# Kernel tuning notes

Measured on AMD Instinct MI355X. Metric: run time of the kernel, lower is better.

The kernel has to match this reference:

```python
import jax, jax.numpy as jnp
import numpy as np

EPS_BN = 1e-5
K_INTERP = 8
K_NEIGH = 16


def _bn(x, g, b):
    # BatchNorm1d in training mode: batch stats over rows (biased var), eps=1e-5
    m = x.mean(axis=0)
    v = x.var(axis=0)
    return (x - m) * jax.lax.rsqrt(v + EPS_BN) * g + b


def _dist(a, b):
    # a:(B,N,3), b:(B,M,3) -> Euclidean distance (B,N,M), computed via the
    # quadratic expansion (clamped at 0) instead of materializing (B,N,M,3)
    d2 = (jnp.sum(a * a, -1)[:, :, None] + jnp.sum(b * b, -1)[:, None, :]
          - 2.0 * jnp.einsum('bnc,bmc->bnm', a, b))
    return jnp.sqrt(jnp.maximum(d2, 0.0))


def _gather(feats, idx):
    # feats:(B,M,C), idx:(B,N,K) int -> (B,N,K,C)
    return jax.vmap(lambda f, i: f[i])(feats, idx)


def setup_inputs() -> dict:
    key = jax.random.key(0)
    B, N1, N2, DS, DD, DOUT = 4, 4096, 1024, 128, 64, 256
    ks = jax.random.split(key, 20)
    s = 0.02
    inp = {
        'p1': jax.random.uniform(ks[0], (B * N1, 3), jnp.float32),
        'x1': jax.random.normal(ks[1], (B * N1, DD), jnp.float32),
        'o1': (jnp.arange(B, dtype=jnp.int32) + 1) * N1,
        'p2': jax.random.uniform(ks[2], (B * N2, 3), jnp.float32),
        'x2': jax.random.normal(ks[3], (B * N2, DS), jnp.float32),
        'o2': (jnp.arange(B, dtype=jnp.int32) + 1) * N2,
        'batch_size': B,
        # dense_mlp: Linear(DD,DS) + BN
        'W_dense': jax.random.normal(ks[4], (DD, DS), jnp.float32) * s,
        'b_dense': jnp.zeros((DS,), jnp.float32),
        'g_dense': jnp.ones((DS,), jnp.float32),
        'bt_dense': jnp.zeros((DS,), jnp.float32),
        # CrossAttentionPointTransformerLayer (dim=DS, hidden_mult=1)
        'Wq': jax.random.normal(ks[5], (DS, DS), jnp.float32) * s,
        'Wk': jax.random.normal(ks[6], (DS, DS), jnp.float32) * s,
        'Wv': jax.random.normal(ks[7], (DS, DS), jnp.float32) * s,
        'W1': jax.random.normal(ks[8], (DS, DS), jnp.float32) * s,
        'b1': jnp.zeros((DS,), jnp.float32),
        'g1': jnp.ones((DS,), jnp.float32),
        'bt1': jnp.zeros((DS,), jnp.float32),
        'W2': jax.random.normal(ks[9], (DS, DS), jnp.float32) * s,
        'b2': jnp.zeros((DS,), jnp.float32),
        # output mlp: Linear(DS+DD, DOUT) + BN
        'W_out': jax.random.normal(ks[10], (DS + DD, DOUT), jnp.float32) * s,
        'b_out': jnp.zeros((DOUT,), jnp.float32),
        'g_out': jnp.ones((DOUT,), jnp.float32),
        'bt_out': jnp.zeros((DOUT,), jnp.float32),
    }
    return inp


def reference(p1, x1, o1, p2, x2, o2, batch_size,
              W_dense, b_dense, g_dense, bt_dense,
              Wq, Wk, Wv, W1, b1, g1, bt1, W2, b2,
              W_out, b_out, g_out, bt_out):
    B = int(batch_size)
    N1 = p1.shape[0] // B
    N2 = p2.shape[0] // B
    DS = x2.shape[-1]

    # dense_mlp
    x1_dense = jax.nn.relu(_bn(x1 @ W_dense + b_dense, g_dense, bt_dense))  # (B*N1, DS)

    # pointops.interpolation(p2, p1, x2, o2, o1, k=8): inverse-distance kNN interp
    p1b = p1.reshape(B, N1, 3)
    p2b = p2.reshape(B, N2, 3)
    x2b = x2.reshape(B, N2, DS)
    d12 = _dist(p1b, p2b)                       # (B,N1,N2)
    negd, idx = jax.lax.top_k(-d12, K_INTERP)   # k nearest in p2
    dknn = -negd
    recip = 1.0 / (dknn + 1e-8)
    w = recip / recip.sum(-1, keepdims=True)    # (B,N1,8)
    x2_interp = jnp.einsum('bnk,bnkc->bnc', w, _gather(x2b, idx))  # (B,N1,DS)

    # CrossAttentionPointTransformerLayer(x_e=x1_dense, x_r=x_d=x2_interp, pos=p1)
    x_e = x1_dense.reshape(B, N1, DS)
    q = x_e @ Wq
    k = x2_interp @ Wk
    v = x2_interp @ Wv
    rel_dist = _dist(p1b, p1b)                  # (B,N1,N1)
    _, nidx = jax.lax.top_k(-rel_dist, K_NEIGH) # 16 nearest neighbors
    kg = _gather(k, nidx)                        # (B,N1,16,DS)
    vg = _gather(v, nidx)
    xeg = _gather(x_e, nidx)
    qk_rel = q[:, :, None, :] - kg
    v2 = vg + xeg
    h = (qk_rel + xeg).reshape(-1, DS)           # (B*N1*16, DS)
    h = jax.nn.relu(_bn(h @ W1 + b1, g1, bt1))
    sim = (h @ W2 + b2).reshape(B, N1, K_NEIGH, DS)
    attn = jax.nn.softmax(sim, axis=-2)          # over neighbors
    agg = jnp.einsum('bnkc,bnkc->bnc', attn, v2).reshape(B * N1, DS)

    # output mlp
    x = jax.nn.relu(_bn(jnp.concatenate([agg, x1], axis=-1) @ W_out + b_out,
                        g_out, bt_out))
    return (p1, x, o1)
```

## Files before the change

kernel.cpp:

```cpp
#include <hip/hip_runtime.h>
#include <math.h>

#define BB 4
#define NN1 4096
#define NN2 1024
#define DS 128
#define DD 64
#define DOUT 256
#define M1 16384
#define MH 262144
#define KCAT 192
#define KI 8
#define KN 16

#define OUT_P1 49152
#define OUT_X  49152
#define OUT_O1 4243456


static const size_t OFF_WTS  = 16777216;
static const size_t OFF_TMP  = 33554432;
static const size_t OFF_XD   = OFF_TMP  + 2097152;
static const size_t OFF_XI   = OFF_XD   + 2097152;
static const size_t OFF_Q    = OFF_XI   + 2097152;
static const size_t OFF_K    = OFF_Q    + 2097152;
static const size_t OFF_V    = OFF_K    + 2097152;
static const size_t OFF_OUTP = OFF_V    + 2097152;
static const size_t OFF_NIDX = OFF_OUTP + 4194304;
static const size_t OFF_STAT = OFF_NIDX + 262144;
static const size_t OFF_P1Q  = OFF_STAT + 4096;
static const size_t OFF_P2Q  = OFF_P1Q  + 65536;
static const size_t OFF_P1S  = OFF_P2Q  + 16384;
static const size_t OFF_P2S  = OFF_P1S  + 65536;

#define WDH 0
#define WDL 8192
#define WQH 16384
#define WQL 32768
#define WKH 49152
#define WKL 65536
#define WVH 81920
#define WVL 98304
#define W1H 114688
#define W1L 131072
#define W2H 147456
#define W2L 163840
#define WOH 180224
#define WOL 229376

typedef __attribute__((ext_vector_type(8))) short short8;
typedef __attribute__((ext_vector_type(4))) float floatx4;
typedef __attribute__((ext_vector_type(2))) float float2v;

__device__ inline unsigned short f2bf(float f) {
    union { float f; unsigned int u; } x; x.f = f;
    unsigned int r = x.u + 0x7fffu + ((x.u >> 16) & 1u);
    return (unsigned short)(r >> 16);
}
__device__ inline float bf2f(unsigned short h) {
    union { unsigned int u; float f; } x; x.u = ((unsigned int)h) << 16;
    return x.f;
}
__device__ inline unsigned long long shfl_xor_u64(unsigned long long v, int m) {
    unsigned lo = (unsigned)v, hi = (unsigned)(v >> 32);
    lo = (unsigned)__shfl_xor((int)lo, m);
    hi = (unsigned)__shfl_xor((int)hi, m);
    return ((unsigned long long)hi << 32) | lo;
}
__device__ inline unsigned cvt_pk_bf16(float lo, float hi) {
    unsigned r;
    asm volatile("v_cvt_pk_bf16_f32 %0, %1, %2" : "=v"(r) : "v"(lo), "v"(hi));
    return r;
}

#define PRO_STAT  (OUT_P1 + BB)
#define PRO_PACK  (PRO_STAT + 3072)
#define PRO_TOTAL (PRO_PACK + M1 + BB*NN2)
#define NPRO 285
struct SwzParams {
    const float* W[7];
    unsigned short* hi[7];
    unsigned short* lo[7];
    int N[7];
    int fid0[8];
};
__global__ __launch_bounds__(256) void k_prolog(
    const float* __restrict__ p1, const int* __restrict__ o1,
    const float* __restrict__ p2, float* __restrict__ out,
    float* __restrict__ stat, float4* __restrict__ p1q,
    float4* __restrict__ p2q, float* __restrict__ p1s,
    float* __restrict__ p2s, SwzParams p)
{
    if (blockIdx.x < NPRO) {
        int i = blockIdx.x * 256 + threadIdx.x;
        if (i < OUT_P1) out[i] = p1[i];
        else if (i < PRO_STAT) out[OUT_O1 + (i - OUT_P1)] = (float)o1[i - OUT_P1];
        else if (i < PRO_PACK) stat[i - PRO_STAT] = 0.f;
        else if (i < PRO_TOTAL) {
            int j = i - PRO_PACK;
            const float* src; float4* dst; float* ps; int jj;
            if (j < M1) { src = p1; dst = p1q; ps = p1s; jj = j; }
            else        { src = p2; dst = p2q; ps = p2s; jj = j - M1; }
            float x = src[jj*3+0] * 16384.f;
            float y = src[jj*3+1] * 16384.f;
            float z = src[jj*3+2] * 16384.f;
            float n = fmaf(z, z, fmaf(y, y, x*x));
            dst[jj] = make_float4(x, y, z, n);
            int pb8 = (jj >> 1)*8 + (jj & 1);
            ps[pb8]   = x + x; ps[pb8+2] = y + y;
            ps[pb8+4] = z + z; ps[pb8+6] = n;
        }
        return;
    }
    int fid = (blockIdx.x - NPRO)*4 + (threadIdx.x >> 6);
    int lane = threadIdx.x & 63;
    if (fid >= 272) return;
    int seg = 0;
    #pragma unroll
    for (int i = 1; i < 7; i++) if (fid >= p.fid0[i]) seg = i;
    int f = fid - p.fid0[seg];
    const float* W = p.W[seg];
    int N = p.N[seg];
    int ncj = N >> 4;
    int slab = f / ncj, cj = f - slab*ncj;
    int n  = cj*16 + (lane & 15);
    int k0 = slab*32 + (lane >> 4)*8;
    unsigned int oh[8], ol[8];
    #pragma unroll
    for (int j = 0; j < 8; j++) {
        float v = W[(size_t)(k0 + j) * N + n];
        unsigned short h = f2bf(v);
        oh[j] = h;
        ol[j] = f2bf(v - bf2f(h));
    }
    uint4 ph, pl;
    ph.x = oh[0] | (oh[1] << 16); ph.y = oh[2] | (oh[3] << 16);
    ph.z = oh[4] | (oh[5] << 16); ph.w = oh[6] | (oh[7] << 16);
    pl.x = ol[0] | (ol[1] << 16); pl.y = ol[2] | (ol[3] << 16);
    pl.z = ol[4] | (ol[5] << 16); pl.w = ol[6] | (ol[7] << 16);
    ((uint4*)p.hi[seg])[f*64 + lane] = ph;
    ((uint4*)p.lo[seg])[f*64 + lane] = pl;
}

template<int N, int K, int MODE, int STATS, int BNA, int NSPL>
__global__ __launch_bounds__(256) void k_gemm_mf(
    const float* __restrict__ Amat, const unsigned short* __restrict__ Whi,
    const unsigned short* __restrict__ Wlo, const float* __restrict__ bias,
    float* __restrict__ C, const float* __restrict__ aux,
    float* __restrict__ sums, float* __restrict__ sumsq,
    const float* __restrict__ bsums, const float* __restrict__ bsumsq,
    const float* __restrict__ bg, const float* __restrict__ bbt)
{
    constexpr int ncj  = N >> 4;
    constexpr int ncjL = ncj / NSPL;
    constexpr int NL   = ncjL * 16;
    __shared__ float sstat[STATS ? 2*NL : 1];
    __shared__ float sbn[BNA ? 2*DS : 1];
    const int t = threadIdx.x, w = t >> 6, lane = t & 63;
    const int quad = lane >> 4, c = lane & 15;
    const int row = blockIdx.x*64 + w*16 + c;
    const int sA = (MODE == 2) ? DS : K;
    constexpr int nslab = K >> 5;
    const int seg = (MODE == 3) ? blockIdx.y : 0;
    const int yn  = (MODE == 3) ? blockIdx.z : blockIdx.y;
    const int cj0 = yn * ncjL;
    const float* Abase = (MODE == 3 && seg > 0) ? aux : Amat;
    const unsigned short* WhiS = Whi + (size_t)seg*32768;
    const unsigned short* WloS = Wlo + (size_t)seg*32768;
    float* CS = C + (size_t)seg*2097152;
    unsigned short* CS16 = (unsigned short*)C + (size_t)seg*4194304;
    if (STATS) {
        for (int i = t; i < 2*NL; i += 256) sstat[i] = 0.f;
    }
    if (BNA) {
        if (t < DS) {
            const float invM = 1.f / (float)M1;
            float m   = bsums[t] * invM;
            float var = bsumsq[t] * invM - m*m;
            float sc  = bg[t] * rsqrtf(var + 1e-5f);
            sbn[t] = sc;
            sbn[DS + t] = bbt[t] - m * sc;
        }
    }
    if (STATS || BNA) __syncthreads();

    floatx4 acc[ncjL];
    #pragma unroll
    for (int cj = 0; cj < ncjL; cj++) acc[cj] = (floatx4){0.f,0.f,0.f,0.f};

    #pragma unroll
    for (int slab = 0; slab < nslab; slab++) {
        const int kk = slab*32 + quad*8;
        const float* src;
        if (MODE == 2 && kk >= DS) src = aux + (size_t)row*DD + (kk - DS);
        else                       src = Abase + (size_t)row*sA + kk;
        floatx4 va = *(const floatx4*)src;
        floatx4 vb = *(const floatx4*)(src + 4);
        if (BNA && MODE == 3 && seg == 0) {
            #pragma unroll
            for (int j = 0; j < 4; j++) {
                va[j] = fmaxf(fmaf(va[j], sbn[kk+j],   sbn[DS+kk+j]),   0.f);
                vb[j] = fmaxf(fmaf(vb[j], sbn[kk+4+j], sbn[DS+kk+4+j]), 0.f);
            }
        }
        short8 ahi, alo;
        #pragma unroll
        for (int j = 0; j < 4; j++) {
            unsigned short h = f2bf(va[j]);
            ahi[j] = (short)h; alo[j] = (short)f2bf(va[j] - bf2f(h));
        }
        #pragma unroll
        for (int j = 0; j < 4; j++) {
            unsigned short h = f2bf(vb[j]);
            ahi[4+j] = (short)h; alo[4+j] = (short)f2bf(vb[j] - bf2f(h));
        }
        const short8* bh = (const short8*)WhiS + (size_t)slab*ncj*64;
        const short8* bl = (const short8*)WloS + (size_t)slab*ncj*64;
        #pragma unroll
        for (int cj = 0; cj < ncjL; cj++) {
            short8 bhv = bh[(cj0 + cj)*64 + lane];
            short8 blv = bl[(cj0 + cj)*64 + lane];
            acc[cj] = __builtin_amdgcn_mfma_f32_16x16x32_bf16(alo, bhv, acc[cj], 0, 0, 0);
            acc[cj] = __builtin_amdgcn_mfma_f32_16x16x32_bf16(ahi, blv, acc[cj], 0, 0, 0);
            acc[cj] = __builtin_amdgcn_mfma_f32_16x16x32_bf16(ahi, bhv, acc[cj], 0, 0, 0);
        }
    }
    const int rbase = blockIdx.x*64 + w*16 + quad*4;
    #pragma unroll
    for (int cj = 0; cj < ncjL; cj++) {
        const int colG = (cj0 + cj)*16 + c;
        const float bb = bias ? bias[colG] : 0.f;
        float s = 0.f, ss = 0.f;
        #pragma unroll
        for (int p = 0; p < 4; p++) {
            float v = acc[cj][p] + bb;
            if (MODE == 3) {
                if (seg > 0) {
                    float xv = Amat[(size_t)(rbase + p)*DS + colG];
                    if (BNA) xv = fmaxf(fmaf(xv, sbn[colG], sbn[DS+colG]), 0.f);
                    if (seg == 1) v = xv - v;
                    else          v += xv;
                }
                CS16[(size_t)(rbase + p)*N + colG] = f2bf(v);
            } else {
                CS[(size_t)(rbase + p)*N + colG] = v;
            }
            if (STATS) { s += v; ss += v*v; }
        }
        if (STATS) {
            s  += __shfl_xor(s, 16);  s  += __shfl_xor(s, 32);
            ss += __shfl_xor(ss, 16); ss += __shfl_xor(ss, 32);
            if (quad == 0) {
                atomicAdd(&sstat[cj*16 + c], s);
                atomicAdd(&sstat[NL + cj*16 + c], ss);
            }
        }
    }
    if (STATS) {
        __syncthreads();
        for (int i = t; i < NL; i += 256) {
            atomicAdd(&sums[cj0*16 + i],  sstat[i]);
            atomicAdd(&sumsq[cj0*16 + i], sstat[NL + i]);
        }
    }
}

__global__ __launch_bounds__(256) void k_gemm_qe(
    const unsigned short* __restrict__ q16, const unsigned short* __restrict__ e16,
    const unsigned short* __restrict__ W1hi, const float* __restrict__ b1,
    unsigned short* __restrict__ qw, unsigned short* __restrict__ ew)
{
    const int t = threadIdx.x, w = t >> 6, lane = t & 63;
    const int quad = lane >> 4, c = lane & 15;
    const int y = blockIdx.y;
    const int cj0 = blockIdx.z * 4;
    const unsigned short* A = y ? e16 : q16;
    unsigned short* C16 = y ? ew : qw;
    const int row = blockIdx.x*64 + w*16 + c;

    floatx4 acc[4];
    #pragma unroll
    for (int cj = 0; cj < 4; cj++) acc[cj] = (floatx4){0.f,0.f,0.f,0.f};

    #pragma unroll
    for (int slab = 0; slab < 4; slab++) {
        uint4 av = *(const uint4*)(A + (size_t)row*DS + slab*32 + quad*8);
        short8 af;
        ((uint4*)&af)[0] = av;
        const short8* bh = (const short8*)W1hi + (size_t)slab*8*64;
        #pragma unroll
        for (int cj = 0; cj < 4; cj++) {
            short8 bhv = bh[(cj0 + cj)*64 + lane];
            acc[cj] = __builtin_amdgcn_mfma_f32_16x16x32_bf16(af, bhv, acc[cj], 0, 0, 0);
        }
    }
    const int rbase = blockIdx.x*64 + w*16 + quad*4;
    #pragma unroll
    for (int cj = 0; cj < 4; cj++) {
        const int colG = (cj0 + cj)*16 + c;
        const float bb = y ? b1[colG] : 0.f;
        #pragma unroll
        for (int p = 0; p < 4; p++)
            C16[(size_t)(rbase + p)*DS + colG] = f2bf(acc[cj][p] + bb);
    }
}

__global__ __launch_bounds__(256) void k_hstat(
    const unsigned short* __restrict__ qw, const unsigned short* __restrict__ ew,
    const int* __restrict__ nidx,
    float* __restrict__ sums, float* __restrict__ sumsq)
{
    __shared__ float sstat[256];
    const int t = threadIdx.x, w = t >> 6, lane = t & 63;
    sstat[t] = 0.f;
    __syncthreads();
    const int col = lane*2;
    float Sx = 0.f, Sy = 0.f, SSx = 0.f, SSy = 0.f;
    #pragma unroll
    for (int g2 = 0; g2 < 4; g2++) {
        const int gp = blockIdx.x*16 + w*4 + g2;
        unsigned av = *(const unsigned*)(qw + (size_t)gp*DS + col);
        float ax = bf2f((unsigned short)(av & 0xffffu));
        float ay = bf2f((unsigned short)(av >> 16));
        float B1x = 0.f, B1y = 0.f, B2x = 0.f, B2y = 0.f;
        const int* np = nidx + gp*16;
        #pragma unroll
        for (int cc = 0; cc < 16; cc++) {
            int m = np[cc];
            unsigned bv = *(const unsigned*)(ew + (size_t)m*DS + col);
            float bx = bf2f((unsigned short)(bv & 0xffffu));
            float by = bf2f((unsigned short)(bv >> 16));
            B1x += bx; B1y += by;
            B2x = fmaf(bx, bx, B2x); B2y = fmaf(by, by, B2y);
        }
        Sx += fmaf(16.f, ax, B1x);
        Sy += fmaf(16.f, ay, B1y);
        SSx += fmaf(16.f*ax, ax, fmaf(2.f*ax, B1x, B2x));
        SSy += fmaf(16.f*ay, ay, fmaf(2.f*ay, B1y, B2y));
    }
    atomicAdd(&sstat[col],       Sx); atomicAdd(&sstat[col+1],       Sy);
    atomicAdd(&sstat[128 + col], SSx); atomicAdd(&sstat[128 + col+1], SSy);
    __syncthreads();
    if (t < 128) atomicAdd(&sums[t], sstat[t]);
    else         atomicAdd(&sumsq[t - 128], sstat[t]);
}

__global__ __launch_bounds__(256) void k_attn3(
    const unsigned short* __restrict__ qw, const unsigned short* __restrict__ ew,
    const float* __restrict__ sums_h, const float* __restrict__ sumsq_h,
    const float* __restrict__ g1, const float* __restrict__ bt1,
    const unsigned short* __restrict__ W2sw,
    const unsigned short* __restrict__ v, const int* __restrict__ nidx,
    float* __restrict__ agg)
{
    __shared__ unsigned short WF[16384];
    __shared__ float s_sc[DS], s_sh[DS];
    const int t = threadIdx.x;
    #pragma unroll
    for (int i = 0; i < 8; i++)
        ((uint4*)WF)[t + 256*i] = ((const uint4*)W2sw)[t + 256*i];
    if (t < DS) {
        const float invM = 1.f / (float)MH;
        float m   = sums_h[t] * invM;
        float var = sumsq_h[t] * invM - m*m;
        float sc  = g1[t] * rsqrtf(var + 1e-5f);
        s_sc[t] = sc;
        s_sh[t] = bt1[t] - m * sc;
    }
    __syncthreads();

    const int w = t >> 6, lane = t & 63;
    const int gp = blockIdx.x * 4 + w;
    const int quad = lane >> 4, c = lane & 15;
    const int mrow = nidx[gp*16 + c];

    floatx4 acc[8];
    #pragma unroll
    for (int cj = 0; cj < 8; cj++) acc[cj] = (floatx4){0.f, 0.f, 0.f, 0.f};

    for (int ks = 0; ks < 4; ks++) {
        const int ko = ks*32 + quad*8;
        uint4 qv4 = *(const uint4*)(qw + (size_t)gp*DS + ko);
        uint4 ev4 = *(const uint4*)(ew + (size_t)mrow*DS + ko);
        floatx4 sc0 = *(const floatx4*)&s_sc[ko];
        floatx4 sc1 = *(const floatx4*)&s_sc[ko + 4];
        floatx4 sh0 = *(const floatx4*)&s_sh[ko];
        floatx4 sh1 = *(const floatx4*)&s_sh[ko + 4];
        unsigned qwv[4] = {qv4.x, qv4.y, qv4.z, qv4.w};
        unsigned ewv[4] = {ev4.x, ev4.y, ev4.z, ev4.w};
        short8 af;
        #pragma unroll
        for (int j = 0; j < 4; j++) {
            float h0 = bf2f((unsigned short)(qwv[j] & 0xffffu))
                     + bf2f((unsigned short)(ewv[j] & 0xffffu));
            float h1 = bf2f((unsigned short)(qwv[j] >> 16))
                     + bf2f((unsigned short)(ewv[j] >> 16));
            float f0 = fmaxf(fmaf(h0, (j<2)?sc0[2*j]:sc1[2*j-4],   (j<2)?sh0[2*j]:sh1[2*j-4]),   0.f);
            float f1 = fmaxf(fmaf(h1, (j<2)?sc0[2*j+1]:sc1[2*j-3], (j<2)?sh0[2*j+1]:sh1[2*j-3]), 0.f);
            ((unsigned*)&af)[j] = cvt_pk_bf16(f0, f1);
        }
        #pragma unroll
        for (int cj = 0; cj < 8; cj++) {
            short8 bfv = ((const short8*)WF)[(ks*8 + cj)*64 + lane];
            acc[cj] = __builtin_amdgcn_mfma_f32_16x16x32_bf16(af, bfv, acc[cj], 0, 0, 0);
        }
    }

    int nid[4];
    #pragma unroll
    for (int p = 0; p < 4; p++) nid[p] = nidx[gp*16 + quad*4 + p];

    #pragma unroll
    for (int cj = 0; cj < 8; cj++) {
        float m4 = fmaxf(fmaxf(acc[cj][0], acc[cj][1]), fmaxf(acc[cj][2], acc[cj][3]));
        m4 = fmaxf(m4, __shfl_xor(m4, 16));
        m4 = fmaxf(m4, __shfl_xor(m4, 32));
        float e[4]; float s4 = 0.f;
        #pragma unroll
        for (int p = 0; p < 4; p++) { e[p] = __expf(acc[cj][p] - m4); s4 += e[p]; }
        s4 += __shfl_xor(s4, 16); s4 += __shfl_xor(s4, 32);
        const float inv = 1.f / s4;
        const int col = cj*16 + c;
        float a = 0.f;
        #pragma unroll
        for (int p = 0; p < 4; p++)
            a = fmaf(e[p]*inv, bf2f(v[(size_t)nid[p]*DS + col]), a);
        a += __shfl_xor(a, 16); a += __shfl_xor(a, 32);
        if (quad == 0) agg[(size_t)gp*DS + col] = a;
    }
}

__global__ __launch_bounds__(256) void k_bnrelu(
    const float4* __restrict__ X, const float* __restrict__ sums,
    const float* __restrict__ sumsq, const float* __restrict__ g,
    const float* __restrict__ bt, float invM,
    float4* __restrict__ Y, size_t total4, int N)
{
    size_t i = (size_t)blockIdx.x * 256 + threadIdx.x;
    if (i < total4) {
        int c = (int)((i*4) & (size_t)(N - 1));
        float4 sm = *(const float4*)(sums + c);
        float4 sq = *(const float4*)(sumsq + c);
        float4 gg = *(const float4*)(g + c);
        float4 bb = *(const float4*)(bt + c);
        float4 x = X[i], y;
        float m0 = sm.x*invM, m1 = sm.y*invM, m2 = sm.z*invM, m3 = sm.w*invM;
        float s0 = gg.x*rsqrtf(sq.x*invM - m0*m0 + 1e-5f);
        float s1 = gg.y*rsqrtf(sq.y*invM - m1*m1 + 1e-5f);
        float s2 = gg.z*rsqrtf(sq.z*invM - m2*m2 + 1e-5f);
        float s3 = gg.w*rsqrtf(sq.w*invM - m3*m3 + 1e-5f);
        y.x = fmaxf(fmaf(x.x, s0, bb.x - m0*s0), 0.f);
        y.y = fmaxf(fmaf(x.y, s1, bb.y - m1*s1), 0.f);
        y.z = fmaxf(fmaf(x.z, s2, bb.z - m2*s2), 0.f);
        y.w = fmaxf(fmaf(x.w, s3, bb.w - m3*s3), 0.f);
        Y[i] = y;
    }
}

template<int NCAND, int KSEL, int EPI, int CAP>
__device__ __forceinline__ void sel_body(
    int gp0,
    const float4* __restrict__ qpts4, const float4* __restrict__ cpts4,
    const float* __restrict__ cpairs,
    int* __restrict__ nidx, const float* __restrict__ x2, float* __restrict__ xi,
    unsigned* hist0, unsigned* hist1,
    unsigned* skey, unsigned* sidx,
    float* swtE, unsigned* sidxE,
    unsigned* wpart, int* sstate)
{
    const int b = gp0 >> 12;
    const int t = threadIdx.x, wv = t >> 6, lane = t & 63;
    constexpr int ITER  = NCAND / 256;
    constexpr int PITER = NCAND / 512;

    const float4 qv0 = qpts4[gp0];
    const float4 qv1 = qpts4[gp0 + 1];
    const float4* pb = cpts4 + (size_t)b*NCAND;
    const float*  pbs = cpairs + (size_t)b*NCAND*4;

    unsigned kreg[2][ITER];
    if (t < 16)      ((uint4*)hist0)[t]      = (uint4){0u,0u,0u,0u};
    else if (t < 32) ((uint4*)hist1)[t - 16] = (uint4){0u,0u,0u,0u};
    __syncthreads();

    {
        const float2v nqx0 = {-qv0.x, -qv0.x}, nqy0 = {-qv0.y, -qv0.y};
        const float2v nqz0 = {-qv0.z, -qv0.z}, qw0 = {qv0.w, qv0.w};
        const float2v nqx1 = {-qv1.x, -qv1.x}, nqy1 = {-qv1.y, -qv1.y};
        const float2v nqz1 = {-qv1.z, -qv1.z}, qw1 = {qv1.w, qv1.w};
        #pragma unroll
        for (int pi = 0; pi < PITER; pi++) {
            const int ip = t + 256*pi;
            float4 A  = ((const float4*)pbs)[2*ip];
            float4 Bv = ((const float4*)pbs)[2*ip + 1];
            float2v xp = {A.x, A.y},  yp = {A.z, A.w};
            float2v zp = {Bv.x, Bv.y}, wp = {Bv.z, Bv.w};
            float2v d0 = wp + qw0;
            d0 = __builtin_elementwise_fma(xp, nqx0, d0);
            d0 = __builtin_elementwise_fma(yp, nqy0, d0);
            d0 = __builtin_elementwise_fma(zp, nqz0, d0);
            float2v d1 = wp + qw1;
            d1 = __builtin_elementwise_fma(xp, nqx1, d1);
            d1 = __builtin_elementwise_fma(yp, nqy1, d1);
            d1 = __builtin_elementwise_fma(zp, nqz1, d1);
            unsigned ka = (unsigned)d0[0], kb = (unsigned)d0[1];
            unsigned kc = (unsigned)d1[0], kd = (unsigned)d1[1];
            kreg[0][2*pi] = ka; kreg[0][2*pi+1] = kb;
            kreg[1][2*pi] = kc; kreg[1][2*pi+1] = kd;
            if ((ka >> 20) < CAP) atomicAdd(&hist0[ka >> 20], 1u);
            if ((kb >> 20) < CAP) atomicAdd(&hist0[kb >> 20], 1u);
            if ((kc >> 20) < CAP) atomicAdd(&hist1[kc >> 20], 1u);
            if ((kd >> 20) < CAP) atomicAdd(&hist1[kd >> 20], 1u);
        }
    }
    __syncthreads();

    if (wv < 2) {
        unsigned* H = wv ? hist1 : hist0;
        unsigned h = (lane < CAP) ? H[lane] : 0u;
        unsigned incl = h;
        #pragma unroll
        for (int off = 1; off < 64; off <<= 1) {
            unsigned o = (unsigned)__shfl_up((int)incl, off);
            if (lane >= off) incl += o;
        }
        unsigned excl = incl - h;
        const int base = wv*8;
        if ((int)excl < KSEL && KSEL <= (int)(excl + h)) {
            sstate[base+0] = lane; sstate[base+1] = (int)excl; sstate[base+2] = (int)h;
            sstate[base+3] = ((int)(excl + h) <= 64) ? 1 : 0;
            sstate[base+4] = 0;
        }
        unsigned tot = (unsigned)__shfl((int)incl, 63);
        if (lane == 0 && (int)tot < KSEL) sstate[base+3] = -1;
    }
    __syncthreads();

    if (sstate[3] == -1 || sstate[11] == -1) {
        for (int qi = 0; qi < 2; qi++) {
            if (sstate[qi*8+3] != -1) continue;
            ((uint4*)hist0)[t] = (uint4){0u,0u,0u,0u};
            __syncthreads();
            #pragma unroll
            for (int it = 0; it < ITER; it++)
                atomicAdd(&hist0[kreg[qi][it] >> 20], 1u);
            __syncthreads();
            uint4 h4 = ((const uint4*)hist0)[t];
            unsigned hv[4] = {h4.x, h4.y, h4.z, h4.w};
            unsigned tsum = hv[0]+hv[1]+hv[2]+hv[3];
            unsigned incl = tsum;
            #pragma unroll
            for (int off = 1; off < 64; off <<= 1) {
                unsigned o = (unsigned)__shfl_up((int)incl, off);
                if (lane >= off) incl += o;
            }
            if (lane == 63) wpart[wv] = incl;
            __syncthreads();
            unsigned wbase = 0;
            for (int i2 = 0; i2 < wv; i2++) wbase += wpart[i2];
            unsigned excl = wbase + incl - tsum;
            if ((int)excl < KSEL && KSEL <= (int)(excl + tsum)) {
                unsigned cum = excl;
                #pragma unroll
                for (int i2 = 0; i2 < 4; i2++) {
                    unsigned h = hv[i2];
                    if ((int)cum < KSEL && KSEL <= (int)(cum + h)) {
                        sstate[qi*8+0] = t*4 + i2; sstate[qi*8+1] = (int)cum;
                        sstate[qi*8+2] = (int)h;
                        sstate[qi*8+3] = ((int)cum + (int)h <= 64) ? 1 : 0;
                        sstate[qi*8+4] = 0;
                        break;
                    }
                    cum += h;
                }
            }
            __syncthreads();
        }
    }

    if (sstate[3] == 1 && sstate[11] == 1) {
        const unsigned P0 = (unsigned)sstate[0];
        const unsigned P1 = (unsigned)sstate[8];
        #pragma unroll
        for (int pi = 0; pi < PITER; pi++) {
            const int ip = t + 256*pi;
            #pragma unroll
            for (int c2 = 0; c2 < 2; c2++) {
                const int j = 2*ip + c2;
                const unsigned k0 = kreg[0][2*pi+c2], k1 = kreg[1][2*pi+c2];
                if ((k0 >> 20) <= P0) {
                    int pos = (int)atomicAdd((unsigned*)&sstate[4], 1u);
                    skey[pos] = k0; sidx[pos] = (unsigned)j;
                }
                if ((k1 >> 20) <= P1) {
                    int pos = (int)atomicAdd((unsigned*)&sstate[12], 1u);
                    skey[64 + pos] = k1; sidx[64 + pos] = (unsigned)j;
                }
            }
        }
    } else {
        #pragma unroll
        for (int qi = 0; qi < 2; qi++) {
            const float4 qv = qi ? qv1 : qv0;
            unsigned P = (unsigned)sstate[qi*8+0];
            int S = sstate[qi*8+1], cntB = sstate[qi*8+2], mode = sstate[qi*8+3];
            int gsh = 20;
            if (mode == 0) {
                for (int round = 1; round < 4; round++) {
                    const int nb  = (round == 3) ? 16 : 256;
                    const int wb  = (round == 3) ? 4 : 8;
                    const int sh  = (round == 1) ? 12 : (round == 2 ? 4 : 0);
                    const int psh = sh + wb;
                    if (t < nb) hist0[t] = 0u;
                    __syncthreads();
                    #pragma unroll
                    for (int it = 0; it < ITER; it++) {
                        unsigned key = kreg[qi][it];
                        if ((key >> psh) == P)
                            atomicAdd(&hist0[(key >> sh) & (nb - 1)], 1u);
                    }
                    __syncthreads();
                    unsigned hv = (t < nb) ? hist0[t] : 0u;
                    unsigned tsum = hv;
                    unsigned incl = tsum;
                    #pragma unroll
                    for (int off = 1; off < 64; off <<= 1) {
                        unsigned o = (unsigned)__shfl_up((int)incl, off);
                        if (lane >= off) incl += o;
                    }
                    if (lane == 63) wpart[wv] = incl;
                    __syncthreads();
                    unsigned wbase = 0;
                    for (int i2 = 0; i2 < wv; i2++) wbase += wpart[i2];
                    unsigned exclT = wbase + incl - tsum;
                    const int need = KSEL - S;
                    if ((int)exclT < need && need <= (int)(exclT + tsum)) {
                        int Snew = S + (int)exclT;
                        int tot  = Snew + (int)tsum;
                        sstate[qi*8+0] = (int)((P << wb) | (unsigned)t);
                        sstate[qi*8+1] = Snew; sstate[qi*8+2] = (int)tsum;
                        sstate[qi*8+3] = (tot <= 64) ? 1 : ((round == 3) ? 2 : 0);
                        sstate[qi*8+4] = 0;
                    }
                    __syncthreads();
                    P = (unsigned)sstate[qi*8+0]; S = sstate[qi*8+1];
                    cntB = sstate[qi*8+2]; mode = sstate[qi*8+3];
                    gsh = sh;
                    if (mode) break;
                }
            }
            if (mode == 1) {
                #pragma unroll
                for (int pi = 0; pi < PITER; pi++) {
                    const int ip = t + 256*pi;
                    #pragma unroll
                    for (int c2 = 0; c2 < 2; c2++) {
                        const int j = 2*ip + c2;
                        unsigned key = kreg[qi][2*pi+c2];
                        if ((key >> gsh) <= P) {
                            int pos = (int)atomicAdd((unsigned*)&sstate[qi*8+4], 1u);
                            skey[qi*64 + pos] = key; sidx[qi*64 + pos] = (unsigned)j;
                        }
                    }
                }
            } else if (mode != 1) {
                if (t < 64) {
                    const unsigned long long lmask = (1ull << lane) - 1ull;
                    int cnt = 0;
                    for (int pass = 0; pass < 2; pass++) {
                        for (int it = 0; it < NCAND/64; it++) {
                            int j = lane + 64*it;
                            float4 cv = pb[j];
                            float dot = fmaf(qv.z, cv.z, fmaf(qv.y, cv.y, qv.x*cv.x));
                            float d2 = fmaxf(fmaf(-2.f, dot, qv.w + cv.w), 0.f);
                            unsigned key = (unsigned)d2;
                            bool f = pass ? (key == P) : (key < P);
                            unsigned long long bal = __ballot(f);
                            if (f) {
                                int pos = cnt + __popcll(bal & lmask);
                                if (pos < 64) { skey[qi*64 + pos] = key; sidx[qi*64 + pos] = (unsigned)j; }
                            }
                            cnt += __popcll(bal);
                        }
                    }
                    if (lane == 0) { sstate[qi*8+1] = min(cnt, 64); sstate[qi*8+2] = 0; }
                }
            }
            __syncthreads();
        }
    }
    __syncthreads();

    if (wv < 2) {
        const int q = wv;
        const int total = sstate[q*8+1] + sstate[q*8+2];
        unsigned long long v = ~0ull;
        if (lane < total)
            v = (((unsigned long long)skey[q*64 + lane]) << 32) | sidx[q*64 + lane];
        #pragma unroll
        for (int k = 2; k <= 64; k <<= 1) {
            #pragma unroll
            for (int jj = k >> 1; jj > 0; jj >>= 1) {
                unsigned long long p = shfl_xor_u64(v, jj);
                bool up = ((lane & k) == 0);
                bool takeMin = (((lane & jj) == 0) == up);
                bool pl = p < v;
                v = (takeMin == pl) ? p : v;
            }
        }
        if (EPI == 0) {
            if (lane < KSEL)
                nidx[(gp0 + q)*KSEL + lane] = b*NCAND + (int)(v & 0xffffffffull);
        } else {
            const float4 qq = q ? qv1 : qv0;
            float wgt = 0.f;
            unsigned si = (unsigned)(v & 0xffffffffull);
            if (lane < KSEL) {
                float4 cv = pb[si];
                float dot = fmaf(qq.z, cv.z, fmaf(qq.y, cv.y, qq.x*cv.x));
                float d2 = fmaxf(fmaf(-2.f, dot, qq.w + cv.w), 0.f);
                wgt = 1.f / (sqrtf(d2) + 1.6384e-4f);
            }
            float ws = wgt;
            ws += __shfl_xor(ws, 1); ws += __shfl_xor(ws, 2); ws += __shfl_xor(ws, 4);
            if (lane < KSEL) {
                swtE[q*KSEL + lane]  = wgt / ws;
                sidxE[q*KSEL + lane] = si;
            }
        }
    }

    if (EPI == 1) {
        __syncthreads();
        const int qi2 = t >> 7, tt = t & 127;
        const float* x2b = x2 + (size_t)b*NCAND*DS;
        float a = 0.f;
        #pragma unroll
        for (int r = 0; r < KSEL; r++)
            a = fmaf(swtE[qi2*KSEL + r], x2b[(size_t)sidxE[qi2*KSEL + r]*DS + tt], a);
        xi[(size_t)(gp0 + qi2)*DS + tt] = a;
    }
}

__global__ __launch_bounds__(256) void k_sel2(
    const float4* __restrict__ p1q, const float4* __restrict__ p2q,
    const float* __restrict__ p1s, const float* __restrict__ p2s,
    int* __restrict__ nidx, const float* __restrict__ x2, float* __restrict__ xi)
{
    __shared__ __align__(16) unsigned hist0[1024], hist1[1024];
    __shared__ __align__(16) unsigned skey[128], sidx[128];
    __shared__ float    swtE[2*KI];
    __shared__ unsigned sidxE[2*KI];
    __shared__ unsigned wpart[8];
    __shared__ int      sstate[20];
    const int bid = blockIdx.x;
    if (bid < M1/2) {
        sel_body<NN1, KN, 0, 32>(bid*2, p1q, p1q, p1s, nidx, nullptr, nullptr,
                                 hist0, hist1, skey, sidx, swtE, sidxE, wpart, sstate);
    } else {
        sel_body<NN2, KI, 1, 64>((bid - M1/2)*2, p1q, p2q, p2s, nullptr, x2, xi,
                                 hist0, hist1, skey, sidx, swtE, sidxE, wpart, sstate);
    }
}

extern "C" void kernel_launch(void* const* d_in, const int* in_sizes, int n_in,
                              void* d_out, int out_size, void* d_ws, size_t ws_size,
                              hipStream_t stream)
{
    const float* p1 = (const float*)d_in[0];
    const float* x1 = (const float*)d_in[1];
    const int*   o1 = (const int*)d_in[2];
    const float* p2 = (const float*)d_in[3];
    const float* x2 = (const float*)d_in[4];
    const float* W_dense = (const float*)d_in[7];
    const float* b_dense = (const float*)d_in[8];
    const float* g_dense = (const float*)d_in[9];
    const float* bt_dense= (const float*)d_in[10];
    const float* Wq = (const float*)d_in[11];
    const float* Wk = (const float*)d_in[12];
    const float* Wv = (const float*)d_in[13];
    const float* W1 = (const float*)d_in[14];
    const float* b1 = (const float*)d_in[15];
    const float* g1 = (const float*)d_in[16];
    const float* bt1= (const float*)d_in[17];
    const float* W2 = (const float*)d_in[18];
    const float* W_out = (const float*)d_in[20];
    const float* b_out = (const float*)d_in[21];
    const float* g_out = (const float*)d_in[22];
    const float* bt_out= (const float*)d_in[23];

    float* ws   = (float*)d_ws;
    unsigned short* wts  = (unsigned short*)(ws + OFF_WTS);
    float* tmp  = ws + OFF_TMP;
    float* xi   = ws + OFF_XI;
    float* qm   = ws + OFF_Q;
    float* outp = ws + OFF_OUTP;
    int*   nidx = (int*)(ws + OFF_NIDX);
    float* stat = ws + OFF_STAT;
    float4* p1q = (float4*)(ws + OFF_P1Q);
    float4* p2q = (float4*)(ws + OFF_P2Q);
    float* p1s = ws + OFF_P1S;
    float* p2s = ws + OFF_P2S;
    unsigned short* q16 = (unsigned short*)(ws + OFF_Q);
    unsigned short* e16 = (unsigned short*)(ws + OFF_K);
    unsigned short* v16 = (unsigned short*)(ws + OFF_V);
    unsigned short* qw16 = (unsigned short*)(ws + OFF_XD);
    unsigned short* ew16 = (unsigned short*)(ws + OFF_OUTP);
    float* sums_d = stat,      *sumsq_d = stat+256;
    float* sums_h = stat+1024, *sumsq_h = stat+1280;
    float* sums_o = stat+2048, *sumsq_o = stat+2304;
    float* out = (float*)d_out;

    SwzParams sp;
    sp.W[0]=W_dense; sp.W[1]=Wq; sp.W[2]=Wk; sp.W[3]=Wv; sp.W[4]=W1; sp.W[5]=W2; sp.W[6]=W_out;
    sp.hi[0]=wts+WDH; sp.hi[1]=wts+WQH; sp.hi[2]=wts+WKH; sp.hi[3]=wts+WVH;
    sp.hi[4]=wts+W1H; sp.hi[5]=wts+W2H; sp.hi[6]=wts+WOH;
    sp.lo[0]=wts+WDL; sp.lo[1]=wts+WQL; sp.lo[2]=wts+WKL; sp.lo[3]=wts+WVL;
    sp.lo[4]=wts+W1L; sp.lo[5]=wts+W2L; sp.lo[6]=wts+WOL;
    sp.N[0]=128; sp.N[1]=128; sp.N[2]=128; sp.N[3]=128; sp.N[4]=128; sp.N[5]=128; sp.N[6]=256;
    sp.fid0[0]=0; sp.fid0[1]=16; sp.fid0[2]=48; sp.fid0[3]=80; sp.fid0[4]=112;
    sp.fid0[5]=144; sp.fid0[6]=176; sp.fid0[7]=272;
    k_prolog<<<NPRO + 68, 256, 0, stream>>>(p1, o1, p2, out, stat, p1q, p2q, p1s, p2s, sp);

    k_sel2<<<M1, 256, 0, stream>>>(p1q, p2q, p1s, p2s, nidx, x2, xi);

    k_gemm_mf<128,64,0,1,0,2><<<dim3(M1/64,2), 256, 0, stream>>>(x1, wts+WDH, wts+WDL,
        b_dense, tmp, nullptr, sums_d, sumsq_d, nullptr, nullptr, nullptr, nullptr);

    k_gemm_mf<128,128,3,0,1,2><<<dim3(M1/64,3,2), 256, 0, stream>>>(tmp, wts+WQH, wts+WQL,
        nullptr, qm, xi, nullptr, nullptr, sums_d, sumsq_d, g_dense, bt_dense);

    k_gemm_qe<<<dim3(M1/64, 2, 2), 256, 0, stream>>>(q16, e16, wts+W1H, b1, qw16, ew16);
    k_hstat<<<M1/16, 256, 0, stream>>>(qw16, ew16, nidx, sums_h, sumsq_h);

    k_attn3<<<M1/4, 256, 0, stream>>>(qw16, ew16, sums_h, sumsq_h, g1, bt1,
        wts+W2H, v16, nidx, tmp);

    k_gemm_mf<256,192,2,1,0,4><<<dim3(M1/64,4), 256, 0, stream>>>(tmp, wts+WOH, wts+WOL,
        b_out, outp, x1, sums_o, sumsq_o, nullptr, nullptr, nullptr, nullptr);
    k_bnrelu<<<(M1*DOUT/4)/256, 256, 0, stream>>>((const float4*)outp, sums_o, sumsq_o,
        g_out, bt_out, 1.f/(float)M1, (float4*)(out + OUT_X), (size_t)M1*DOUT/4, DOUT);
}
```

Measured before the change: 297.6 us.

## Pool candidate keys during histogram pass and split GEMMs across more column blocks

During the first histogram pass, the selection kernel now appends candidates whose top bucket falls under a smaller cap into a shared-memory pool. The later gather step then scans only this pool instead of rescanning every register key. The histogram caps are halved, which makes fallback refinement more likely. Separately, the QE, Q/K/V and output GEMMs are launched with more column-split blocks, so each block holds fewer accumulators and the grid is larger. The pool adds shared atomics in the hot pass and extra LDS use, which can lower occupancy.

```diff
diff --git a/kernel.cpp b/kernel.cpp
--- a/kernel.cpp
+++ b/kernel.cpp
@@ -12,6 +12,7 @@
 #define KCAT 192
 #define KI 8
 #define KN 16
+#define POOLCAP 512
 
 #define OUT_P1 49152
 #define OUT_X  49152
@@ -273,14 +274,14 @@
     const int t = threadIdx.x, w = t >> 6, lane = t & 63;
     const int quad = lane >> 4, c = lane & 15;
     const int y = blockIdx.y;
-    const int cj0 = blockIdx.z * 4;
+    const int cj0 = blockIdx.z * 2;
     const unsigned short* A = y ? e16 : q16;
     unsigned short* C16 = y ? ew : qw;
     const int row = blockIdx.x*64 + w*16 + c;
 
-    floatx4 acc[4];
-    #pragma unroll
-    for (int cj = 0; cj < 4; cj++) acc[cj] = (floatx4){0.f,0.f,0.f,0.f};
+    floatx4 acc[2];
+    #pragma unroll
+    for (int cj = 0; cj < 2; cj++) acc[cj] = (floatx4){0.f,0.f,0.f,0.f};
 
     #pragma unroll
     for (int slab = 0; slab < 4; slab++) {
@@ -289,14 +290,14 @@
         ((uint4*)&af)[0] = av;
         const short8* bh = (const short8*)W1hi + (size_t)slab*8*64;
         #pragma unroll
-        for (int cj = 0; cj < 4; cj++) {
+        for (int cj = 0; cj < 2; cj++) {
             short8 bhv = bh[(cj0 + cj)*64 + lane];
             acc[cj] = __builtin_amdgcn_mfma_f32_16x16x32_bf16(af, bhv, acc[cj], 0, 0, 0);
         }
     }
     const int rbase = blockIdx.x*64 + w*16 + quad*4;
     #pragma unroll
-    for (int cj = 0; cj < 4; cj++) {
+    for (int cj = 0; cj < 2; cj++) {
         const int colG = (cj0 + cj)*16 + c;
         const float bb = y ? b1[colG] : 0.f;
         #pragma unroll
@@ -465,6 +466,7 @@
     int* __restrict__ nidx, const float* __restrict__ x2, float* __restrict__ xi,
     unsigned* hist0, unsigned* hist1,
     unsigned* skey, unsigned* sidx,
+    unsigned* pkey, unsigned* pidxp,
     float* swtE, unsigned* sidxE,
     unsigned* wpart, int* sstate)
 {
@@ -481,6 +483,7 @@
     unsigned kreg[2][ITER];
     if (t < 16)      ((uint4*)hist0)[t]      = (uint4){0u,0u,0u,0u};
     else if (t < 32) ((uint4*)hist1)[t - 16] = (uint4){0u,0u,0u,0u};
+    if (t < 2) { sstate[t*8+5] = 0; sstate[t*8+6] = 0; }
     __syncthreads();
 
     {
@@ -503,14 +506,23 @@
             d1 = __builtin_elementwise_fma(xp, nqx1, d1);
             d1 = __builtin_elementwise_fma(yp, nqy1, d1);
             d1 = __builtin_elementwise_fma(zp, nqz1, d1);
-            unsigned ka = (unsigned)d0[0], kb = (unsigned)d0[1];
-            unsigned kc = (unsigned)d1[0], kd = (unsigned)d1[1];
-            kreg[0][2*pi] = ka; kreg[0][2*pi+1] = kb;
-            kreg[1][2*pi] = kc; kreg[1][2*pi+1] = kd;
-            if ((ka >> 20) < CAP) atomicAdd(&hist0[ka >> 20], 1u);
-            if ((kb >> 20) < CAP) atomicAdd(&hist0[kb >> 20], 1u);
-            if ((kc >> 20) < CAP) atomicAdd(&hist1[kc >> 20], 1u);
-            if ((kd >> 20) < CAP) atomicAdd(&hist1[kd >> 20], 1u);
+            unsigned kk[4];
+            kk[0] = (unsigned)d0[0]; kk[1] = (unsigned)d0[1];
+            kk[2] = (unsigned)d1[0]; kk[3] = (unsigned)d1[1];
+            kreg[0][2*pi] = kk[0]; kreg[0][2*pi+1] = kk[1];
+            kreg[1][2*pi] = kk[2]; kreg[1][2*pi+1] = kk[3];
+            #pragma unroll
+            for (int c2 = 0; c2 < 4; c2++) {
+                const int qi = c2 >> 1;
+                if ((kk[c2] >> 20) < CAP) {
+                    atomicAdd((qi ? hist1 : hist0) + (kk[c2] >> 20), 1u);
+                    int pp = (int)atomicAdd((unsigned*)&sstate[qi*8+5], 1u);
+                    if (pp < POOLCAP) {
+                        pkey[qi*POOLCAP + pp]  = kk[c2];
+                        pidxp[qi*POOLCAP + pp] = (unsigned)(2*ip + (c2 & 1));
+                    }
+                }
+            }
         }
     }
     __syncthreads();
@@ -539,6 +551,7 @@
     if (sstate[3] == -1 || sstate[11] == -1) {
         for (int qi = 0; qi < 2; qi++) {
             if (sstate[qi*8+3] != -1) continue;
+            if (t == 0) sstate[qi*8+6] = 1;
             ((uint4*)hist0)[t] = (uint4){0u,0u,0u,0u};
             __syncthreads();
             #pragma unroll
@@ -578,116 +591,103 @@
         }
     }
 
-    if (sstate[3] == 1 && sstate[11] == 1) {
-        const unsigned P0 = (unsigned)sstate[0];
-        const unsigned P1 = (unsigned)sstate[8];
-        #pragma unroll
-        for (int pi = 0; pi < PITER; pi++) {
-            const int ip = t + 256*pi;
-            #pragma unroll
-            for (int c2 = 0; c2 < 2; c2++) {
-                const int j = 2*ip + c2;
-                const unsigned k0 = kreg[0][2*pi+c2], k1 = kreg[1][2*pi+c2];
-                if ((k0 >> 20) <= P0) {
-                    int pos = (int)atomicAdd((unsigned*)&sstate[4], 1u);
-                    skey[pos] = k0; sidx[pos] = (unsigned)j;
+    #pragma unroll
+    for (int qi = 0; qi < 2; qi++) {
+        const float4 qv = qi ? qv1 : qv0;
+        unsigned P = (unsigned)sstate[qi*8+0];
+        int S = sstate[qi*8+1], cntB = sstate[qi*8+2], mode = sstate[qi*8+3];
+        const bool usePool = (sstate[qi*8+6] == 0) && (sstate[qi*8+5] <= POOLCAP);
+        int gsh = 20;
+        if (mode == 0) {
+            for (int round = 1; round < 4; round++) {
+                const int nb  = (round == 3) ? 16 : 256;
+                const int wb  = (round == 3) ? 4 : 8;
+                const int sh  = (round == 1) ? 12 : (round == 2 ? 4 : 0);
+                const int psh = sh + wb;
+                if (t < nb) hist0[t] = 0u;
+                __syncthreads();
+                #pragma unroll
+                for (int it = 0; it < ITER; it++) {
+                    unsigned key = kreg[qi][it];
+                    if ((key >> psh) == P)
+                        atomicAdd(&hist0[(key >> sh) & (nb - 1)], 1u);
                 }
-                if ((k1 >> 20) <= P1) {
-                    int pos = (int)atomicAdd((unsigned*)&sstate[12], 1u);
-                    skey[64 + pos] = k1; sidx[64 + pos] = (unsigned)j;
+                __syncthreads();
+                unsigned hv = (t < nb) ? hist0[t] : 0u;
+                unsigned tsum = hv;
+                unsigned incl = tsum;
+                #pragma unroll
+                for (int off = 1; off < 64; off <<= 1) {
+                    unsigned o = (unsigned)__shfl_up((int)incl, off);
+                    if (lane >= off) incl += o;
                 }
-            }
-        }
-    } else {
-        #pragma unroll
-        for (int qi = 0; qi < 2; qi++) {
-            const float4 qv = qi ? qv1 : qv0;
-            unsigned P = (unsigned)sstate[qi*8+0];
-            int S = sstate[qi*8+1], cntB = sstate[qi*8+2], mode = sstate[qi*8+3];
-            int gsh = 20;
-            if (mode == 0) {
-                for (int round = 1; round < 4; round++) {
-                    const int nb  = (round == 3) ? 16 : 256;
-                    const int wb  = (round == 3) ? 4 : 8;
-                    const int sh  = (round == 1) ? 12 : (round == 2 ? 4 : 0);
-                    const int psh = sh + wb;
-                    if (t < nb) hist0[t] = 0u;
-                    __syncthreads();
-                    #pragma unroll
-                    for (int it = 0; it < ITER; it++) {
-                        unsigned key = kreg[qi][it];
-                        if ((key >> psh) == P)
-                            atomicAdd(&hist0[(key >> sh) & (nb - 1)], 1u);
-                    }
-                    __syncthreads();
-                    unsigned hv = (t < nb) ? hist0[t] : 0u;
-                    unsigned tsum = hv;
-                    unsigned incl = tsum;
-                    #pragma unroll
-                    for (int off = 1; off < 64; off <<= 1) {
-                        unsigned o = (unsigned)__shfl_up((int)incl, off);
-                        if (lane >= off) incl += o;
-                    }
-                    if (lane == 63) wpart[wv] = incl;
-                    __syncthreads();
-                    unsigned wbase = 0;
-                    for (int i2 = 0; i2 < wv; i2++) wbase += wpart[i2];
-                    unsigned exclT = wbase + incl - tsum;
-                    const int need = KSEL - S;
-                    if ((int)exclT < need && need <= (int)(exclT + tsum)) {
-                        int Snew = S + (int)exclT;
-                        int tot  = Snew + (int)tsum;
-                        sstate[qi*8+0] = (int)((P << wb) | (unsigned)t);
-                        sstate[qi*8+1] = Snew; sstate[qi*8+2] = (int)tsum;
-                        sstate[qi*8+3] = (tot <= 64) ? 1 : ((round == 3) ? 2 : 0);
-                        sstate[qi*8+4] = 0;
-                    }
-                    __syncthreads();
-                    P = (unsigned)sstate[qi*8+0]; S = sstate[qi*8+1];
-                    cntB = sstate[qi*8+2]; mode = sstate[qi*8+3];
-                    gsh = sh;
-                    if (mode) break;
+                if (lane == 63) wpart[wv] = incl;
+                __syncthreads();
+                unsigned wbase = 0;
+                for (int i2 = 0; i2 < wv; i2++) wbase += wpart[i2];
+                unsigned exclT = wbase + incl - tsum;
+                const int need = KSEL - S;
+                if ((int)exclT < need && need <= (int)(exclT + tsum)) {
+                    int Snew = S + (int)exclT;
+                    int tot  = Snew + (int)tsum;
+                    sstate[qi*8+0] = (int)((P << wb) | (unsigned)t);
+                    sstate[qi*8+1] = Snew; sstate[qi*8+2] = (int)tsum;
+                    sstate[qi*8+3] = (tot <= 64) ? 1 : ((round == 3) ? 2 : 0);
+                    sstate[qi*8+4] = 0;
                 }
-            }
-            if (mode == 1) {
-                #pragma unroll
-                for (int pi = 0; pi < PITER; pi++) {
-                    const int ip = t + 256*pi;
-                    #pragma unroll
-                    for (int c2 = 0; c2 < 2; c2++) {
-                        const int j = 2*ip + c2;
-                        unsigned key = kreg[qi][2*pi+c2];
-                        if ((key >> gsh) <= P) {
-                            int pos = (int)atomicAdd((unsigned*)&sstate[qi*8+4], 1u);
-                            skey[qi*64 + pos] = key; sidx[qi*64 + pos] = (unsigned)j;
-                        }
+                __syncthreads();
+                P = (unsigned)sstate[qi*8+0]; S = sstate[qi*8+1];
+                cntB = sstate[qi*8+2]; mode = sstate[qi*8+3];
+                gsh = sh;
+                if (mode) break;
+            }
+        }
+        if (mode == 1) {
+            if (usePool) {
+                const int pcnt = sstate[qi*8+5];
+                for (int i = t; i < pcnt; i += 256) {
+                    unsigned key = pkey[qi*POOLCAP + i];
+                    if ((key >> gsh) <= P) {
+                        int pos = (int)atomicAdd((unsigned*)&sstate[qi*8+4], 1u);
+                        skey[qi*64 + pos] = key; sidx[qi*64 + pos] = pidxp[qi*POOLCAP + i];
                     }
                 }
-            } else if (mode != 1) {
-                if (t < 64) {
-                    const unsigned long long lmask = (1ull << lane) - 1ull;
-                    int cnt = 0;
-                    for (int pass = 0; pass < 2; pass++) {
-                        for (int it = 0; it < NCAND/64; it++) {
-                            int j = lane + 64*it;
-                            float4 cv = pb[j];
-                            float dot = fmaf(qv.z, cv.z, fmaf(qv.y, cv.y, qv.x*cv.x));
-                            float d2 = fmaxf(fmaf(-2.f, dot, qv.w + cv.w), 0.f);
-                            unsigned key = (unsigned)d2;
-                            bool f = pass ? (key == P) : (key < P);
-                            unsigned long long bal = __ballot(f);
-                            if (f) {
-                                int pos = cnt + __popcll(bal & lmask);
-                                if (pos < 64) { skey[qi*64 + pos] = key; sidx[qi*64 + pos] = (unsigned)j; }
-                            }
-                            cnt += __popcll(bal);
+            } else {
+                #pragma unroll
+                for (int it = 0; it < ITER; it++) {
+                    const int j = t + 256*((it & 1) ? (it >> 1) + PITER : (it >> 1));
+                    unsigned key = kreg[qi][it];
+                    const int jj = 2*(t + 256*(it >> 1)) + (it & 1);
+                    if ((key >> gsh) <= P) {
+                        int pos = (int)atomicAdd((unsigned*)&sstate[qi*8+4], 1u);
+                        skey[qi*64 + pos] = key; sidx[qi*64 + pos] = (unsigned)jj;
+                    }
+                }
+            }
+        } else if (mode == 2) {
+            if (t < 64) {
+                const unsigned long long lmask = (1ull << lane) - 1ull;
+                int cnt = 0;
+                for (int pass = 0; pass < 2; pass++) {
+                    for (int it = 0; it < NCAND/64; it++) {
+                        int j = lane + 64*it;
+                        float4 cv = pb[j];
+                        float dot = fmaf(qv.z, cv.z, fmaf(qv.y, cv.y, qv.x*cv.x));
+                        float d2 = fmaxf(fmaf(-2.f, dot, qv.w + cv.w), 0.f);
+                        unsigned key = (unsigned)d2;
+                        bool f = pass ? (key == P) : (key < P);
+                        unsigned long long bal = __ballot(f);
+                        if (f) {
+                            int pos = cnt + __popcll(bal & lmask);
+                            if (pos < 64) { skey[qi*64 + pos] = key; sidx[qi*64 + pos] = (unsigned)j; }
                         }
+                        cnt += __popcll(bal);
                     }
-                    if (lane == 0) { sstate[qi*8+1] = min(cnt, 64); sstate[qi*8+2] = 0; }
                 }
-            }
-            __syncthreads();
-        }
+                if (lane == 0) { sstate[qi*8+1] = min(cnt, 64); sstate[qi*8+2] = 0; }
+            }
+        }
+        __syncthreads();
     }
     __syncthreads();
 
@@ -749,17 +749,20 @@
 {
     __shared__ __align__(16) unsigned hist0[1024], hist1[1024];
     __shared__ __align__(16) unsigned skey[128], sidx[128];
+    __shared__ __align__(16) unsigned pkey[2*POOLCAP], pidxp[2*POOLCAP];
     __shared__ float    swtE[2*KI];
     __shared__ unsigned sidxE[2*KI];
     __shared__ unsigned wpart[8];
     __shared__ int      sstate[20];
     const int bid = blockIdx.x;
     if (bid < M1/2) {
-        sel_body<NN1, KN, 0, 32>(bid*2, p1q, p1q, p1s, nidx, nullptr, nullptr,
-                                 hist0, hist1, skey, sidx, swtE, sidxE, wpart, sstate);
+        sel_body<NN1, KN, 0, 16>(bid*2, p1q, p1q, p1s, nidx, nullptr, nullptr,
+                                 hist0, hist1, skey, sidx, pkey, pidxp,
+                                 swtE, sidxE, wpart, sstate);
     } else {
-        sel_body<NN2, KI, 1, 64>((bid - M1/2)*2, p1q, p2q, p2s, nullptr, x2, xi,
-                                 hist0, hist1, skey, sidx, swtE, sidxE, wpart, sstate);
+        sel_body<NN2, KI, 1, 32>((bid - M1/2)*2, p1q, p2q, p2s, nullptr, x2, xi,
+                                 hist0, hist1, skey, sidx, pkey, pidxp,
+                                 swtE, sidxE, wpart, sstate);
     }
 }
 
@@ -827,16 +830,16 @@
     k_gemm_mf<128,64,0,1,0,2><<<dim3(M1/64,2), 256, 0, stream>>>(x1, wts+WDH, wts+WDL,
         b_dense, tmp, nullptr, sums_d, sumsq_d, nullptr, nullptr, nullptr, nullptr);
 
-    k_gemm_mf<128,128,3,0,1,2><<<dim3(M1/64,3,2), 256, 0, stream>>>(tmp, wts+WQH, wts+WQL,
+    k_gemm_mf<128,128,3,0,1,4><<<dim3(M1/64,3,4), 256, 0, stream>>>(tmp, wts+WQH, wts+WQL,
         nullptr, qm, xi, nullptr, nullptr, sums_d, sumsq_d, g_dense, bt_dense);
 
-    k_gemm_qe<<<dim3(M1/64, 2, 2), 256, 0, stream>>>(q16, e16, wts+W1H, b1, qw16, ew16);
+    k_gemm_qe<<<dim3(M1/64, 2, 4), 256, 0, stream>>>(q16, e16, wts+W1H, b1, qw16, ew16);
     k_hstat<<<M1/16, 256, 0, stream>>>(qw16, ew16, nidx, sums_h, sumsq_h);
 
     k_attn3<<<M1/4, 256, 0, stream>>>(qw16, ew16, sums_h, sumsq_h, g1, bt1,
         wts+W2H, v16, nidx, tmp);
 
-    k_gemm_mf<256,192,2,1,0,4><<<dim3(M1/64,4), 256, 0, stream>>>(tmp, wts+WOH, wts+WOL,
+    k_gemm_mf<256,192,2,1,0,8><<<dim3(M1/64,8), 256, 0, stream>>>(tmp, wts+WOH, wts+WOL,
         b_out, outp, x1, sums_o, sumsq_o, nullptr, nullptr, nullptr, nullptr);
     k_bnrelu<<<(M1*DOUT/4)/256, 256, 0, stream>>>((const float4*)outp, sums_o, sumsq_o,
         g_out, bt_out, 1.f/(float)M1, (float4*)(out + OUT_X), (size_t)M1*DOUT/4, DOUT);
```

Measured after the change: 322.3 us. 1.08x slower.
